# Kernel tuning notes

Hardware: AMD Instinct MI355X
Metric: run time of the kernel (lower is better)

The kernel has to match this reference:

```python
import jax, jax.numpy as jnp
import numpy as np

NUM_GROUPS = 8
EPS = 1e-5


def setup_inputs() -> dict:
    key = jax.random.key(0)
    ks = jax.random.split(key, 4)
    C = 128
    x = jax.random.normal(ks[0], (4, C, 64, 64), dtype=jnp.float32)
    gn_weight = jnp.ones((C,), dtype=jnp.float32)
    gn_bias = jnp.zeros((C,), dtype=jnp.float32)
    qkv_weight = jax.random.normal(ks[1], (3 * C, C), dtype=jnp.float32) * (C ** -0.5)
    qkv_bias = jnp.zeros((3 * C,), dtype=jnp.float32)
    proj_weight = jax.random.normal(ks[2], (C, C), dtype=jnp.float32) * (C ** -0.5)
    proj_bias = jnp.zeros((C,), dtype=jnp.float32)
    return {
        "x": x,
        "gn_weight": gn_weight,
        "gn_bias": gn_bias,
        "qkv_weight": qkv_weight,
        "qkv_bias": qkv_bias,
        "proj_weight": proj_weight,
        "proj_bias": proj_bias,
    }


def reference(x, gn_weight, gn_bias, qkv_weight, qkv_bias, proj_weight, proj_bias):
    b, c, h, w = x.shape
    scale = c ** (-0.5)

    # GroupNorm(8, c): normalize over (channels_in_group, h, w)
    xg = x.reshape(b, NUM_GROUPS, c // NUM_GROUPS, h, w)
    mean = jnp.mean(xg, axis=(2, 3, 4), keepdims=True)
    var = jnp.var(xg, axis=(2, 3, 4), keepdims=True)
    xn = ((xg - mean) * jax.lax.rsqrt(var + EPS)).reshape(b, c, h, w)
    xn = xn * gn_weight[None, :, None, None] + gn_bias[None, :, None, None]

    # 1x1 conv QKV == channel matmul; flatten spatial to sequence n = h*w
    xn_flat = xn.reshape(b, c, h * w)  # [b, c, n]
    qkv = jnp.einsum('oc,bcn->bno', qkv_weight, xn_flat) + qkv_bias  # [b, n, 3c]
    q, k, v = qkv[..., :c], qkv[..., c:2 * c], qkv[..., 2 * c:]

    # attention: materializes [b, n, n] scores as in original
    attn = jnp.einsum('bnc,bmc->bnm', q, k) * scale
    attn = jax.nn.softmax(attn, axis=-1)
    out = jnp.einsum('bnm,bmc->bnc', attn, v)  # [b, n, c]

    # proj 1x1 conv + residual
    out = jnp.einsum('oc,bnc->bno', proj_weight, out) + proj_bias  # [b, n, c]
    out = out.transpose(0, 2, 1).reshape(b, c, h, w)
    return x + out
```

## Files before the change

### kernel.cpp

```cpp
#include <hip/hip_runtime.h>

#define BATCH 4
#define CCH 128
#define NSP 4096
#define NGRP 8
#define GROUP_ELEMS 65536
#define QSCALE 0.12751744f
#define EPS_GN 1e-5f
#define OPSTRIDE 2097152
#define LPSTRIDE 16384

typedef short s8b __attribute__((ext_vector_type(8)));
typedef float f32x4 __attribute__((ext_vector_type(4)));

static __device__ __forceinline__ short f2bf(float f) {
  union { float f; unsigned u; } v; v.f = f;
  unsigned r = (v.u + 0x7FFFu + ((v.u >> 16) & 1u)) >> 16;
  return (short)r;
}

static __device__ __forceinline__ float bf2f(short s) {
  unsigned u = ((unsigned)(unsigned short)s) << 16;
  float f; __builtin_memcpy(&f, &u, 4); return f;
}

static __device__ __forceinline__ float fexp2(float x) {
#if __has_builtin(__builtin_amdgcn_exp2f)
  return __builtin_amdgcn_exp2f(x);
#else
  return exp2f(x);
#endif
}

static __device__ __forceinline__ f32x4 mfma16(s8b a, s8b b, f32x4 c) {
  return __builtin_amdgcn_mfma_f32_16x16x32_bf16(a, b, c, 0, 0, 0);
}

static __device__ __forceinline__ void async16(const void* g, void* l) {
  __builtin_amdgcn_global_load_lds(
      (const __attribute__((address_space(1))) void*)g,
      (__attribute__((address_space(3))) void*)l, 16, 0, 0);
}

__global__ void gn_stats(const float* __restrict__ x, float* __restrict__ part) {
  int bx = blockIdx.x;
  int ch = bx & 7, bg = bx >> 3;
  const float* base = x + (size_t)bg * GROUP_ELEMS + (size_t)ch * 8192;
  int t = threadIdx.x;
  float s = 0.f, ss = 0.f;
  #pragma unroll
  for (int i = 0; i < 8; ++i) {
    float4 v = *(const float4*)(base + i * 1024 + t * 4);
    s  += v.x + v.y + v.z + v.w;
    ss += v.x * v.x + v.y * v.y + v.z * v.z + v.w * v.w;
  }
  #pragma unroll
  for (int off = 1; off < 64; off <<= 1) {
    s  += __shfl_xor(s, off);
    ss += __shfl_xor(ss, off);
  }
  __shared__ float red[8];
  int w = t >> 6;
  if ((t & 63) == 0) { red[w * 2] = s; red[w * 2 + 1] = ss; }
  __syncthreads();
  if (t == 0) {
    part[bx * 2]     = red[0] + red[2] + red[4] + red[6];
    part[bx * 2 + 1] = red[1] + red[3] + red[5] + red[7];
  }
}

__global__ void gn_apply(const float* __restrict__ x, const float* __restrict__ gw,
                         const float* __restrict__ gb, const float* __restrict__ part,
                         short* __restrict__ xn) {
  int bx = blockIdx.x;
  int ns = bx & 7, g = (bx >> 3) & 7, b = bx >> 6;
  int bg = b * NGRP + g;
  float s = 0.f, ss = 0.f;
  #pragma unroll
  for (int j = 0; j < 8; ++j) {
    s  += part[(bg * 8 + j) * 2];
    ss += part[(bg * 8 + j) * 2 + 1];
  }
  float mean = s * (1.f / GROUP_ELEMS);
  float var  = ss * (1.f / GROUP_ELEMS) - mean * mean;
  float inv  = rsqrtf(var + EPS_GN);
  int t = threadIdx.x;
  int cl = t & 15, n4 = t >> 4;
  int c = g * 16 + cl;
  float ga = gw[c] * inv;
  float be = gb[c] - mean * ga;
  const float* xr = x + (size_t)(b * CCH + c) * NSP;
  short* xo = xn + (size_t)b * NSP * CCH + c;
  #pragma unroll
  for (int i = 0; i < 8; ++i) {
    int n = ns * 512 + i * 64 + n4 * 4;
    float4 v = *(const float4*)(xr + n);
    xo[(size_t)(n + 0) * CCH] = f2bf(v.x * ga + be);
    xo[(size_t)(n + 1) * CCH] = f2bf(v.y * ga + be);
    xo[(size_t)(n + 2) * CCH] = f2bf(v.z * ga + be);
    xo[(size_t)(n + 3) * CCH] = f2bf(v.w * ga + be);
  }
}

__global__ void qk_gemm(const short* __restrict__ xn, const float* __restrict__ Wqkv,
                        const float* __restrict__ bias, short* __restrict__ q,
                        short* __restrict__ k) {
  int bx = blockIdx.x;
  int ot = bx & 3, nt = (bx >> 2) & 63, b = bx >> 8;
  __shared__ short Xl[64][136];
  __shared__ short Wl[64][136];
  int t = threadIdx.x;
  for (int idx = t; idx < 64 * 16; idx += 256) {
    int row = idx >> 4, c8 = idx & 15;
    *(s8b*)&Xl[row][c8 * 8] =
        *(const s8b*)(xn + ((size_t)(b * NSP + nt * 64 + row)) * CCH + c8 * 8);
  }
  for (int idx = t; idx < 64 * 16; idx += 256) {
    int row = idx >> 4, c8 = idx & 15;
    const float* src = Wqkv + (size_t)(ot * 64 + row) * CCH + c8 * 8;
    s8b wv;
    #pragma unroll
    for (int j = 0; j < 8; ++j) wv[j] = f2bf(src[j]);
    *(s8b*)&Wl[row][c8 * 8] = wv;
  }
  __syncthreads();
  int lane = t & 63, w = t >> 6, l15 = lane & 15, quad = lane >> 4;
  s8b a[4];
  #pragma unroll
  for (int kc = 0; kc < 4; ++kc) a[kc] = *(const s8b*)&Xl[w * 16 + l15][kc * 32 + quad * 8];
  #pragma unroll
  for (int o4 = 0; o4 < 4; ++o4) {
    f32x4 acc = {0.f, 0.f, 0.f, 0.f};
    #pragma unroll
    for (int kc = 0; kc < 4; ++kc) {
      s8b bw = *(const s8b*)&Wl[o4 * 16 + l15][kc * 32 + quad * 8];
      acc = mfma16(a[kc], bw, acc);
    }
    int obase = ot * 64 + o4 * 16;
    short* dst = (obase < 128) ? q : k;
    float mulf = (obase < 128) ? QSCALE : 1.0f;
    int oc = obase - ((obase < 128) ? 0 : 128) + l15;
    float bs = bias[obase + l15];
    #pragma unroll
    for (int r = 0; r < 4; ++r) {
      int n = nt * 64 + w * 16 + quad * 4 + r;
      dst[((size_t)(b * NSP + n)) * CCH + oc] = f2bf((acc[r] + bs) * mulf);
    }
  }
}

__global__ void v_gemm(const short* __restrict__ xn, const float* __restrict__ Wqkv,
                       const float* __restrict__ bias, short* __restrict__ vt) {
  int bx = blockIdx.x;
  int ot = bx & 1, nt = (bx >> 1) & 31, b = bx >> 6;
  __shared__ short Xl[128][136];
  __shared__ short Wl[64][136];
  int t = threadIdx.x;
  for (int idx = t; idx < 128 * 16; idx += 256) {
    int row = idx >> 4, c8 = idx & 15;
    *(s8b*)&Xl[row][c8 * 8] =
        *(const s8b*)(xn + ((size_t)(b * NSP + nt * 128 + row)) * CCH + c8 * 8);
  }
  for (int idx = t; idx < 64 * 16; idx += 256) {
    int row = idx >> 4, c8 = idx & 15;
    const float* src = Wqkv + (size_t)(256 + ot * 64 + row) * CCH + c8 * 8;
    s8b wv;
    #pragma unroll
    for (int j = 0; j < 8; ++j) wv[j] = f2bf(src[j]);
    *(s8b*)&Wl[row][c8 * 8] = wv;
  }
  __syncthreads();
  int lane = t & 63, w = t >> 6, l15 = lane & 15, quad = lane >> 4;
  s8b a[4];
  #pragma unroll
  for (int kc = 0; kc < 4; ++kc) a[kc] = *(const s8b*)&Wl[w * 16 + l15][kc * 32 + quad * 8];
  float bs[4];
  #pragma unroll
  for (int r = 0; r < 4; ++r) bs[r] = bias[256 + ot * 64 + w * 16 + quad * 4 + r];
  #pragma unroll
  for (int ntile = 0; ntile < 8; ++ntile) {
    f32x4 acc = {0.f, 0.f, 0.f, 0.f};
    #pragma unroll
    for (int kc = 0; kc < 4; ++kc) {
      s8b bx2 = *(const s8b*)&Xl[ntile * 16 + l15][kc * 32 + quad * 8];
      acc = mfma16(a[kc], bx2, acc);
    }
    #pragma unroll
    for (int r = 0; r < 4; ++r) {
      int og = ot * 64 + w * 16 + quad * 4 + r;
      int n = nt * 128 + ntile * 16 + l15;
      vt[((size_t)(b * CCH + og)) * NSP + n] = f2bf(acc[r] + bs[r]);
    }
  }
}

__global__ __launch_bounds__(256, 2) void flash(const short* __restrict__ q,
                                                const short* __restrict__ k,
                                                const short* __restrict__ vt,
                                                short* __restrict__ Op,
                                                float* __restrict__ Lp) {
  int bx = blockIdx.x;
  int kh = bx & 3, b = (bx >> 2) & 3, qt = bx >> 4;
  __shared__ short Kl[2][64 * 128];
  __shared__ short Vl[2][128 * 64];
  __shared__ short Pl[4][16 * 74];
  int t = threadIdx.x;
  int lane = t & 63, w = t >> 6;
  int l15 = lane & 15, quad = lane >> 4;
  const short* kbase = k + (size_t)b * NSP * CCH;
  const short* vbase = vt + (size_t)b * CCH * NSP;
  int kt0 = kh * 1024;

  int krow_in_chunk = lane >> 4, kgrp = lane & 15;
  int vrow_in_chunk = lane >> 3, vgrp = lane & 7;

  s8b aq[2][4];
  #pragma unroll
  for (int mt = 0; mt < 2; ++mt) {
    const short* qp =
        q + ((size_t)(b * NSP + qt * 128 + w * 32 + mt * 16 + l15)) * CCH + quad * 8;
    #pragma unroll
    for (int kc = 0; kc < 4; ++kc) aq[mt][kc] = *(const s8b*)(qp + kc * 32);
  }
  f32x4 O[2][8];
  float l4[2][4];
  #pragma unroll
  for (int mt = 0; mt < 2; ++mt) {
    #pragma unroll
    for (int cg = 0; cg < 8; ++cg) O[mt][cg] = (f32x4){0.f, 0.f, 0.f, 0.f};
    #pragma unroll
    for (int r = 0; r < 4; ++r) l4[mt][r] = 0.f;
  }
  short* pw = &Pl[w][0];

  #define STAGE(buf_, key0_)                                                        \
    {                                                                               \
      const int key0v = (key0_);                                                    \
      _Pragma("unroll") for (int si = 0; si < 4; ++si) {                            \
        int c = w * 4 + si;                                                         \
        int rt = c * 4 + krow_in_chunk;                                             \
        async16(kbase + (size_t)(key0v + rt) * CCH + ((kgrp ^ (rt & 15)) * 8),      \
                &Kl[buf_][c * 512]);                                                \
        int rc = c * 8 + vrow_in_chunk;                                             \
        async16(vbase + (size_t)rc * NSP + key0v + ((vgrp ^ (rc & 7)) * 8),         \
                &Vl[buf_][c * 512]);                                                \
      }                                                                             \
    }

  STAGE(0, kt0)
  __syncthreads();

  for (int i = 0; i < 16; ++i) {
    int buf = i & 1;
    if (i < 15) STAGE(buf ^ 1, kt0 + (i + 1) * 64)

    f32x4 s[2][4];
    #pragma unroll
    for (int g2 = 0; g2 < 4; ++g2) {
      const short* kp = &Kl[buf][(g2 * 16 + l15) * 128];
      s8b bk[4];
      #pragma unroll
      for (int kc = 0; kc < 4; ++kc)
        bk[kc] = *(const s8b*)&kp[((kc * 4 + quad) ^ l15) * 8];
      #pragma unroll
      for (int mt = 0; mt < 2; ++mt) {
        f32x4 acc = {0.f, 0.f, 0.f, 0.f};
        acc = mfma16(aq[mt][0], bk[0], acc);
        acc = mfma16(aq[mt][1], bk[1], acc);
        acc = mfma16(aq[mt][2], bk[2], acc);
        acc = mfma16(aq[mt][3], bk[3], acc);
        s[mt][g2] = acc;
      }
    }
    s8b vf[8][2];
    #pragma unroll
    for (int cg = 0; cg < 8; ++cg) {
      const short* vp = &Vl[buf][(cg * 16 + l15) * 64];
      vf[cg][0] = *(const s8b*)&vp[((quad) ^ (l15 & 7)) * 8];
      vf[cg][1] = *(const s8b*)&vp[((4 + quad) ^ (l15 & 7)) * 8];
    }
    #pragma unroll
    for (int mt = 0; mt < 2; ++mt) {
      #pragma unroll
      for (int g2 = 0; g2 < 4; ++g2) {
        #pragma unroll
        for (int r = 0; r < 4; ++r) {
          float p = fexp2(s[mt][g2][r]);
          l4[mt][r] += p;
          unsigned u; __builtin_memcpy(&u, &p, 4);
          pw[(quad * 4 + r) * 74 + g2 * 16 + l15] = (short)((u + 0x8000u) >> 16);
        }
      }
      s8b pf0 = *(const s8b*)&pw[l15 * 74 + quad * 8];
      s8b pf1 = *(const s8b*)&pw[l15 * 74 + 32 + quad * 8];
      #pragma unroll
      for (int cg = 0; cg < 8; ++cg) {
        O[mt][cg] = mfma16(pf0, vf[cg][0], O[mt][cg]);
        O[mt][cg] = mfma16(pf1, vf[cg][1], O[mt][cg]);
      }
    }
    __syncthreads();
  }

  #pragma unroll
  for (int off = 1; off < 16; off <<= 1)
    #pragma unroll
    for (int mt = 0; mt < 2; ++mt)
      #pragma unroll
      for (int r = 0; r < 4; ++r) l4[mt][r] += __shfl_xor(l4[mt][r], off);

  short* ob = Op + (size_t)kh * OPSTRIDE + ((size_t)(b * NSP + qt * 128)) * CCH;
  float* lp = Lp + kh * LPSTRIDE + b * NSP + qt * 128;
  #pragma unroll
  for (int mt = 0; mt < 2; ++mt) {
    #pragma unroll
    for (int r = 0; r < 4; ++r) {
      int n = w * 32 + mt * 16 + quad * 4 + r;
      if (l15 == 0) lp[n] = l4[mt][r];
      #pragma unroll
      for (int cg = 0; cg < 8; ++cg)
        ob[(size_t)n * CCH + cg * 16 + l15] = f2bf(O[mt][cg][r]);
    }
  }
}

__global__ void proj_gemm(const short* __restrict__ Op, const float* __restrict__ Lp,
                          const float* __restrict__ Wp, const float* __restrict__ pbias,
                          const float* __restrict__ x, float* __restrict__ out) {
  int bx = blockIdx.x;
  int nt = bx & 63, b = bx >> 6;
  __shared__ short Wl[128][136];
  int t = threadIdx.x;
  for (int idx = t; idx < 128 * 16; idx += 256) {
    int row = idx >> 4, c8 = idx & 15;
    const float* src = Wp + (size_t)row * CCH + c8 * 8;
    s8b wv;
    #pragma unroll
    for (int j = 0; j < 8; ++j) wv[j] = f2bf(src[j]);
    *(s8b*)&Wl[row][c8 * 8] = wv;
  }
  __syncthreads();
  int lane = t & 63, w = t >> 6, l15 = lane & 15, quad = lane >> 4;
  int row = nt * 64 + w * 16 + l15;
  float lsum = Lp[0 * LPSTRIDE + b * NSP + row] + Lp[1 * LPSTRIDE + b * NSP + row] +
               Lp[2 * LPSTRIDE + b * NSP + row] + Lp[3 * LPSTRIDE + b * NSP + row];
  float linv = 1.f / lsum;
  const short* ap = Op + ((size_t)(b * NSP + row)) * CCH + quad * 8;
  s8b bfr[4];
  #pragma unroll
  for (int kc = 0; kc < 4; ++kc) {
    float acc8[8];
    #pragma unroll
    for (int j = 0; j < 8; ++j) acc8[j] = 0.f;
    #pragma unroll
    for (int s = 0; s < 4; ++s) {
      s8b tv = *(const s8b*)(ap + (size_t)s * OPSTRIDE + kc * 32);
      #pragma unroll
      for (int j = 0; j < 8; ++j) acc8[j] += bf2f(tv[j]);
    }
    #pragma unroll
    for (int j = 0; j < 8; ++j) bfr[kc][j] = f2bf(acc8[j] * linv);
  }
  #pragma unroll
  for (int cg = 0; cg < 8; ++cg) {
    f32x4 acc = {0.f, 0.f, 0.f, 0.f};
    #pragma unroll
    for (int kc = 0; kc < 4; ++kc) {
      s8b aw = *(const s8b*)&Wl[cg * 16 + l15][kc * 32 + quad * 8];
      acc = mfma16(aw, bfr[kc], acc);
    }
    #pragma unroll
    for (int r = 0; r < 4; ++r) {
      int co = cg * 16 + quad * 4 + r;
      int n = nt * 64 + w * 16 + l15;
      size_t off = ((size_t)(b * CCH + co)) * NSP + n;
      out[off] = x[off] + acc[r] + pbias[co];
    }
  }
}

extern "C" void kernel_launch(void* const* d_in, const int* in_sizes, int n_in,
                              void* d_out, int out_size, void* d_ws, size_t ws_size,
                              hipStream_t stream) {
  (void)in_sizes; (void)n_in; (void)out_size; (void)ws_size;
  const float* x    = (const float*)d_in[0];
  const float* gw   = (const float*)d_in[1];
  const float* gb   = (const float*)d_in[2];
  const float* Wqkv = (const float*)d_in[3];
  const float* bqkv = (const float*)d_in[4];
  const float* Wp   = (const float*)d_in[5];
  const float* bp   = (const float*)d_in[6];
  float* out = (float*)d_out;
  char* ws = (char*)d_ws;
  float* part = (float*)ws;
  short* xn    = (short*)(ws + 4096);
  short* q     = (short*)(ws + 4096 + 1ull * 4194304);
  short* k     = (short*)(ws + 4096 + 2ull * 4194304);
  short* vt    = (short*)(ws + 4096 + 3ull * 4194304);
  short* Opart = (short*)(ws + 4096 + 4ull * 4194304);
  float* Lpart = (float*)(ws + 4096 + 8ull * 4194304);

  gn_stats<<<256, 256, 0, stream>>>(x, part);
  gn_apply<<<256, 256, 0, stream>>>(x, gw, gb, part, xn);
  qk_gemm<<<1024, 256, 0, stream>>>(xn, Wqkv, bqkv, q, k);
  v_gemm<<<256, 256, 0, stream>>>(xn, Wqkv, bqkv, vt);
  flash<<<512, 256, 0, stream>>>(q, k, vt, Opart, Lpart);
  proj_gemm<<<256, 256, 0, stream>>>(Opart, Lpart, Wp, bp, x, out);
}
```

Baseline: 149.8 us.

## Merge QK and V projection kernels, pack P stores, compute row sums via MFMA

Combines the QK and V projection GEMMs into one launch by splitting on block index, which removes one kernel launch and lets the two halves overlap. In the flash kernel, softmax probabilities are packed two bf16 values per 32-bit LDS store, and the V-transpose layout is permuted to match. Row sums are now accumulated with an MFMA against a ones vector, replacing per-element adds and the cross-lane shuffle reduction. This spends extra MFMA work and relies on matching the permuted key ordering in both the V layout and the P layout.

```diff
diff --git a/kernel.cpp b/kernel.cpp
--- a/kernel.cpp
+++ b/kernel.cpp
@@ -29,6 +29,17 @@
   return __builtin_amdgcn_exp2f(x);
 #else
   return exp2f(x);
+#endif
+}
+
+static __device__ __forceinline__ unsigned pack2bf(float a, float b) {
+  unsigned ua, ub;
+  __builtin_memcpy(&ua, &a, 4); __builtin_memcpy(&ub, &b, 4);
+  ua += 0x8000u; ub += 0x8000u;
+#if __has_builtin(__builtin_amdgcn_perm)
+  return __builtin_amdgcn_perm(ub, ua, 0x07060302u);
+#else
+  return (ua >> 16) | (ub & 0xFFFF0000u);
 #endif
 }
 
@@ -102,94 +113,92 @@
   }
 }
 
-__global__ void qk_gemm(const short* __restrict__ xn, const float* __restrict__ Wqkv,
-                        const float* __restrict__ bias, short* __restrict__ q,
-                        short* __restrict__ k) {
+__global__ void qkv_gemm(const short* __restrict__ xn, const float* __restrict__ Wqkv,
+                         const float* __restrict__ bias, short* __restrict__ q,
+                         short* __restrict__ k, short* __restrict__ vt) {
+  __shared__ short Xl[128 * 136];
+  __shared__ short Wl[64 * 136];
   int bx = blockIdx.x;
-  int ot = bx & 3, nt = (bx >> 2) & 63, b = bx >> 8;
-  __shared__ short Xl[64][136];
-  __shared__ short Wl[64][136];
   int t = threadIdx.x;
-  for (int idx = t; idx < 64 * 16; idx += 256) {
-    int row = idx >> 4, c8 = idx & 15;
-    *(s8b*)&Xl[row][c8 * 8] =
-        *(const s8b*)(xn + ((size_t)(b * NSP + nt * 64 + row)) * CCH + c8 * 8);
-  }
-  for (int idx = t; idx < 64 * 16; idx += 256) {
-    int row = idx >> 4, c8 = idx & 15;
-    const float* src = Wqkv + (size_t)(ot * 64 + row) * CCH + c8 * 8;
-    s8b wv;
-    #pragma unroll
-    for (int j = 0; j < 8; ++j) wv[j] = f2bf(src[j]);
-    *(s8b*)&Wl[row][c8 * 8] = wv;
-  }
-  __syncthreads();
   int lane = t & 63, w = t >> 6, l15 = lane & 15, quad = lane >> 4;
-  s8b a[4];
-  #pragma unroll
-  for (int kc = 0; kc < 4; ++kc) a[kc] = *(const s8b*)&Xl[w * 16 + l15][kc * 32 + quad * 8];
-  #pragma unroll
-  for (int o4 = 0; o4 < 4; ++o4) {
-    f32x4 acc = {0.f, 0.f, 0.f, 0.f};
-    #pragma unroll
-    for (int kc = 0; kc < 4; ++kc) {
-      s8b bw = *(const s8b*)&Wl[o4 * 16 + l15][kc * 32 + quad * 8];
-      acc = mfma16(a[kc], bw, acc);
-    }
-    int obase = ot * 64 + o4 * 16;
-    short* dst = (obase < 128) ? q : k;
-    float mulf = (obase < 128) ? QSCALE : 1.0f;
-    int oc = obase - ((obase < 128) ? 0 : 128) + l15;
-    float bs = bias[obase + l15];
-    #pragma unroll
-    for (int r = 0; r < 4; ++r) {
-      int n = nt * 64 + w * 16 + quad * 4 + r;
-      dst[((size_t)(b * NSP + n)) * CCH + oc] = f2bf((acc[r] + bs) * mulf);
-    }
-  }
-}
-
-__global__ void v_gemm(const short* __restrict__ xn, const float* __restrict__ Wqkv,
-                       const float* __restrict__ bias, short* __restrict__ vt) {
-  int bx = blockIdx.x;
-  int ot = bx & 1, nt = (bx >> 1) & 31, b = bx >> 6;
-  __shared__ short Xl[128][136];
-  __shared__ short Wl[64][136];
-  int t = threadIdx.x;
-  for (int idx = t; idx < 128 * 16; idx += 256) {
-    int row = idx >> 4, c8 = idx & 15;
-    *(s8b*)&Xl[row][c8 * 8] =
-        *(const s8b*)(xn + ((size_t)(b * NSP + nt * 128 + row)) * CCH + c8 * 8);
-  }
-  for (int idx = t; idx < 64 * 16; idx += 256) {
-    int row = idx >> 4, c8 = idx & 15;
-    const float* src = Wqkv + (size_t)(256 + ot * 64 + row) * CCH + c8 * 8;
-    s8b wv;
-    #pragma unroll
-    for (int j = 0; j < 8; ++j) wv[j] = f2bf(src[j]);
-    *(s8b*)&Wl[row][c8 * 8] = wv;
-  }
-  __syncthreads();
-  int lane = t & 63, w = t >> 6, l15 = lane & 15, quad = lane >> 4;
-  s8b a[4];
-  #pragma unroll
-  for (int kc = 0; kc < 4; ++kc) a[kc] = *(const s8b*)&Wl[w * 16 + l15][kc * 32 + quad * 8];
-  float bs[4];
-  #pragma unroll
-  for (int r = 0; r < 4; ++r) bs[r] = bias[256 + ot * 64 + w * 16 + quad * 4 + r];
-  #pragma unroll
-  for (int ntile = 0; ntile < 8; ++ntile) {
-    f32x4 acc = {0.f, 0.f, 0.f, 0.f};
-    #pragma unroll
-    for (int kc = 0; kc < 4; ++kc) {
-      s8b bx2 = *(const s8b*)&Xl[ntile * 16 + l15][kc * 32 + quad * 8];
-      acc = mfma16(a[kc], bx2, acc);
-    }
-    #pragma unroll
-    for (int r = 0; r < 4; ++r) {
-      int og = ot * 64 + w * 16 + quad * 4 + r;
-      int n = nt * 128 + ntile * 16 + l15;
-      vt[((size_t)(b * CCH + og)) * NSP + n] = f2bf(acc[r] + bs[r]);
+  if (bx < 1024) {
+    int ot = bx & 3, nt = (bx >> 2) & 63, b = bx >> 8;
+    for (int idx = t; idx < 64 * 16; idx += 256) {
+      int row = idx >> 4, c8 = idx & 15;
+      *(s8b*)&Xl[row * 136 + c8 * 8] =
+          *(const s8b*)(xn + ((size_t)(b * NSP + nt * 64 + row)) * CCH + c8 * 8);
+    }
+    for (int idx = t; idx < 64 * 16; idx += 256) {
+      int row = idx >> 4, c8 = idx & 15;
+      const float* src = Wqkv + (size_t)(ot * 64 + row) * CCH + c8 * 8;
+      s8b wv;
+      #pragma unroll
+      for (int j = 0; j < 8; ++j) wv[j] = f2bf(src[j]);
+      *(s8b*)&Wl[row * 136 + c8 * 8] = wv;
+    }
+    __syncthreads();
+    s8b a[4];
+    #pragma unroll
+    for (int kc = 0; kc < 4; ++kc)
+      a[kc] = *(const s8b*)&Xl[(w * 16 + l15) * 136 + kc * 32 + quad * 8];
+    #pragma unroll
+    for (int o4 = 0; o4 < 4; ++o4) {
+      f32x4 acc = {0.f, 0.f, 0.f, 0.f};
+      #pragma unroll
+      for (int kc = 0; kc < 4; ++kc) {
+        s8b bw = *(const s8b*)&Wl[(o4 * 16 + l15) * 136 + kc * 32 + quad * 8];
+        acc = mfma16(a[kc], bw, acc);
+      }
+      int obase = ot * 64 + o4 * 16;
+      short* dst = (obase < 128) ? q : k;
+      float mulf = (obase < 128) ? QSCALE : 1.0f;
+      int oc = obase - ((obase < 128) ? 0 : 128) + l15;
+      float bs = bias[obase + l15];
+      #pragma unroll
+      for (int r = 0; r < 4; ++r) {
+        int n = nt * 64 + w * 16 + quad * 4 + r;
+        dst[((size_t)(b * NSP + n)) * CCH + oc] = f2bf((acc[r] + bs) * mulf);
+      }
+    }
+  } else {
+    int vbx = bx - 1024;
+    int ot = vbx & 1, nt = (vbx >> 1) & 31, b = vbx >> 6;
+    for (int idx = t; idx < 128 * 16; idx += 256) {
+      int row = idx >> 4, c8 = idx & 15;
+      *(s8b*)&Xl[row * 136 + c8 * 8] =
+          *(const s8b*)(xn + ((size_t)(b * NSP + nt * 128 + row)) * CCH + c8 * 8);
+    }
+    for (int idx = t; idx < 64 * 16; idx += 256) {
+      int row = idx >> 4, c8 = idx & 15;
+      const float* src = Wqkv + (size_t)(256 + ot * 64 + row) * CCH + c8 * 8;
+      s8b wv;
+      #pragma unroll
+      for (int j = 0; j < 8; ++j) wv[j] = f2bf(src[j]);
+      *(s8b*)&Wl[row * 136 + c8 * 8] = wv;
+    }
+    __syncthreads();
+    s8b a[4];
+    #pragma unroll
+    for (int kc = 0; kc < 4; ++kc)
+      a[kc] = *(const s8b*)&Wl[(w * 16 + l15) * 136 + kc * 32 + quad * 8];
+    float bs[4];
+    #pragma unroll
+    for (int r = 0; r < 4; ++r) bs[r] = bias[256 + ot * 64 + w * 16 + quad * 4 + r];
+    #pragma unroll
+    for (int ntile = 0; ntile < 8; ++ntile) {
+      f32x4 acc = {0.f, 0.f, 0.f, 0.f};
+      #pragma unroll
+      for (int kc = 0; kc < 4; ++kc) {
+        s8b bx2 = *(const s8b*)&Xl[(ntile * 16 + l15) * 136 + kc * 32 + quad * 8];
+        acc = mfma16(a[kc], bx2, acc);
+      }
+      int g2 = ntile & 3;
+      int npos = nt * 128 + (ntile >> 2) * 64 + l15 * 2 + (g2 & 1) + 32 * (g2 >> 1);
+      #pragma unroll
+      for (int r = 0; r < 4; ++r) {
+        int og = ot * 64 + w * 16 + quad * 4 + r;
+        vt[((size_t)(b * CCH + og)) * NSP + npos] = f2bf(acc[r] + bs[r]);
+      }
     }
   }
 }
@@ -203,7 +212,7 @@
   int kh = bx & 3, b = (bx >> 2) & 3, qt = bx >> 4;
   __shared__ short Kl[2][64 * 128];
   __shared__ short Vl[2][128 * 64];
-  __shared__ short Pl[4][16 * 74];
+  __shared__ short Pl[4][16 * 72];
   int t = threadIdx.x;
   int lane = t & 63, w = t >> 6;
   int l15 = lane & 15, quad = lane >> 4;
@@ -223,14 +232,16 @@
     for (int kc = 0; kc < 4; ++kc) aq[mt][kc] = *(const s8b*)(qp + kc * 32);
   }
   f32x4 O[2][8];
-  float l4[2][4];
+  f32x4 L[2];
   #pragma unroll
   for (int mt = 0; mt < 2; ++mt) {
     #pragma unroll
     for (int cg = 0; cg < 8; ++cg) O[mt][cg] = (f32x4){0.f, 0.f, 0.f, 0.f};
-    #pragma unroll
-    for (int r = 0; r < 4; ++r) l4[mt][r] = 0.f;
-  }
+    L[mt] = (f32x4){0.f, 0.f, 0.f, 0.f};
+  }
+  s8b vone;
+  #pragma unroll
+  for (int j = 0; j < 8; ++j) vone[j] = (short)0x3F80;
   short* pw = &Pl[w][0];
 
   #define STAGE(buf_, key0_)                                                        \
@@ -282,17 +293,18 @@
     #pragma unroll
     for (int mt = 0; mt < 2; ++mt) {
       #pragma unroll
-      for (int g2 = 0; g2 < 4; ++g2) {
-        #pragma unroll
-        for (int r = 0; r < 4; ++r) {
-          float p = fexp2(s[mt][g2][r]);
-          l4[mt][r] += p;
-          unsigned u; __builtin_memcpy(&u, &p, 4);
-          pw[(quad * 4 + r) * 74 + g2 * 16 + l15] = (short)((u + 0x8000u) >> 16);
-        }
-      }
-      s8b pf0 = *(const s8b*)&pw[l15 * 74 + quad * 8];
-      s8b pf1 = *(const s8b*)&pw[l15 * 74 + 32 + quad * 8];
+      for (int r = 0; r < 4; ++r) {
+        float p0 = fexp2(s[mt][0][r]);
+        float p1 = fexp2(s[mt][1][r]);
+        float p2 = fexp2(s[mt][2][r]);
+        float p3 = fexp2(s[mt][3][r]);
+        *(unsigned*)&pw[(quad * 4 + r) * 72 + l15 * 2]      = pack2bf(p0, p1);
+        *(unsigned*)&pw[(quad * 4 + r) * 72 + 32 + l15 * 2] = pack2bf(p2, p3);
+      }
+      s8b pf0 = *(const s8b*)&pw[l15 * 72 + quad * 8];
+      s8b pf1 = *(const s8b*)&pw[l15 * 72 + 32 + quad * 8];
+      L[mt] = mfma16(pf0, vone, L[mt]);
+      L[mt] = mfma16(pf1, vone, L[mt]);
       #pragma unroll
       for (int cg = 0; cg < 8; ++cg) {
         O[mt][cg] = mfma16(pf0, vf[cg][0], O[mt][cg]);
@@ -302,13 +314,6 @@
     __syncthreads();
   }
 
-  #pragma unroll
-  for (int off = 1; off < 16; off <<= 1)
-    #pragma unroll
-    for (int mt = 0; mt < 2; ++mt)
-      #pragma unroll
-      for (int r = 0; r < 4; ++r) l4[mt][r] += __shfl_xor(l4[mt][r], off);
-
   short* ob = Op + (size_t)kh * OPSTRIDE + ((size_t)(b * NSP + qt * 128)) * CCH;
   float* lp = Lp + kh * LPSTRIDE + b * NSP + qt * 128;
   #pragma unroll
@@ -316,7 +321,7 @@
     #pragma unroll
     for (int r = 0; r < 4; ++r) {
       int n = w * 32 + mt * 16 + quad * 4 + r;
-      if (l15 == 0) lp[n] = l4[mt][r];
+      if (l15 == 0) lp[n] = L[mt][r];
       #pragma unroll
       for (int cg = 0; cg < 8; ++cg)
         ob[(size_t)n * CCH + cg * 16 + l15] = f2bf(O[mt][cg][r]);
@@ -402,8 +407,7 @@
 
   gn_stats<<<256, 256, 0, stream>>>(x, part);
   gn_apply<<<256, 256, 0, stream>>>(x, gw, gb, part, xn);
-  qk_gemm<<<1024, 256, 0, stream>>>(xn, Wqkv, bqkv, q, k);
-  v_gemm<<<256, 256, 0, stream>>>(xn, Wqkv, bqkv, vt);
+  qkv_gemm<<<1280, 256, 0, stream>>>(xn, Wqkv, bqkv, q, k, vt);
   flash<<<512, 256, 0, stream>>>(q, k, vt, Opart, Lpart);
   proj_gemm<<<256, 256, 0, stream>>>(Opart, Lpart, Wp, bp, x, out);
 }
```

Result: faster. 135.6 us (-9.4%).
